# Performance work log

Measured on AMD Instinct MI355X. Metric: run time of the kernel, lower is better.

The kernel has to match this reference:

```python
import jax
jax.config.update('jax_enable_x64', True)
import jax.numpy as jnp
import numpy as np

N = 524288
C_IN = 64
C_OUT = 128
GRID = 1024
NB = 4
FILL_KEY = jnp.int64(1) << 62  # pad key, larger than any real packed key


def setup_inputs() -> dict:
    key = jax.random.key(0)
    k1, k2, k3, k4, k5, k6 = jax.random.split(key, 6)
    feat = jax.random.normal(k1, (N, C_IN), dtype=jnp.float32)
    coord = jax.random.uniform(k2, (N, 3), dtype=jnp.float32) * 100.0
    weight = jax.random.normal(k3, (C_OUT, C_IN), dtype=jnp.float32) / np.sqrt(C_IN)
    bias = jax.random.normal(k4, (C_OUT,), dtype=jnp.float32) * 0.01
    grid_coord = jax.random.randint(k5, (N, 3), 0, GRID, dtype=jnp.int64)
    batch = jnp.sort(jax.random.randint(k6, (N,), 0, NB, dtype=jnp.int64))
    return {"feat": feat, "coord": coord, "weight": weight, "bias": bias,
            "grid_coord": grid_coord, "batch": batch, "stride": 2}


def reference(feat, coord, weight, bias, grid_coord, batch, stride):
    n = feat.shape[0]
    g = grid_coord // stride                       # [N,3] int64
    packed = (g[:, 0] + (g[:, 1] << 16) + (g[:, 2] << 32) + (batch << 48))
    # sorted unique keys, padded at the end with FILL_KEY (fixed shape N)
    uniq = jnp.unique(packed, size=n, fill_value=FILL_KEY)
    cluster = jnp.searchsorted(uniq, packed)       # inverse indices [N]
    counts = jax.ops.segment_sum(jnp.ones((n,), jnp.float32), cluster, num_segments=n)
    valid = counts > 0
    # linear projection then max segment-reduce (equiv. to segment_csr 'max')
    proj = feat @ weight.T + bias                  # [N, C_OUT]
    seg_feat = jax.ops.segment_max(proj, cluster, num_segments=n)
    seg_feat = jnp.where(valid[:, None], seg_feat, 0.0)
    # mean segment-reduce of coords
    seg_coord = jax.ops.segment_sum(coord, cluster, num_segments=n)
    seg_coord = seg_coord / jnp.maximum(counts, 1.0)[:, None]
    # decode pooled grid coords and batch from the packed keys
    key_wo_b = jnp.where(valid, uniq % (jnp.int64(1) << 48), 0)
    gx = key_wo_b % (1 << 16)
    gy = (key_wo_b >> 16) % (1 << 16)
    gz = (key_wo_b >> 32) % (1 << 16)
    grid_out = jnp.stack([gx, gy, gz], axis=1)
    batch_out = jnp.where(valid, uniq >> 48, 0)
    return seg_feat, seg_coord, grid_out, batch_out, counts
```

## Files before the change

kernel.cpp:

```cpp
#include <hip/hip_runtime.h>
#include <stdint.h>

#define C_IN 64
#define C_OUT 128
#define NBUCK 32768
#define CAP 64

typedef unsigned int u32;
typedef unsigned long long u64;
typedef __attribute__((ext_vector_type(8))) short bf16x8;
typedef __attribute__((ext_vector_type(4))) float f32x4;

__device__ __forceinline__ bf16x8 cvt8(float4 a, float4 b) {
  union { bf16x8 v; __bf16 h[8]; } r;
  r.h[0] = (__bf16)a.x; r.h[1] = (__bf16)a.y;
  r.h[2] = (__bf16)a.z; r.h[3] = (__bf16)a.w;
  r.h[4] = (__bf16)b.x; r.h[5] = (__bf16)b.y;
  r.h[6] = (__bf16)b.z; r.h[7] = (__bf16)b.w;
  return r.v;
}

__global__ void k0_zero(uint4* __restrict__ p, int n4) {
  int i = blockIdx.x * blockDim.x + threadIdx.x;
  if (i < n4) p[i] = make_uint4(0u, 0u, 0u, 0u);
}

__global__ void k13_scatter(const int* __restrict__ grid, const int* __restrict__ batch,
                            const int* __restrict__ stride, int n,
                            u32* __restrict__ cnt, u64* __restrict__ pairsPad) {
  int q = blockIdx.x * blockDim.x + threadIdx.x;
  int base = q * 4;
  if (base >= n) return;
  int s = stride[0];
  u32 g[12], bt[4];
  if (base + 4 <= n) {
    const int4* g4 = (const int4*)grid;
    int4 ga = g4[q * 3], gb = g4[q * 3 + 1], gc = g4[q * 3 + 2];
    int4 bb = ((const int4*)batch)[q];
    g[0] = ga.x; g[1] = ga.y; g[2] = ga.z; g[3] = ga.w;
    g[4] = gb.x; g[5] = gb.y; g[6] = gb.z; g[7] = gb.w;
    g[8] = gc.x; g[9] = gc.y; g[10] = gc.z; g[11] = gc.w;
    bt[0] = bb.x; bt[1] = bb.y; bt[2] = bb.z; bt[3] = bb.w;
  } else {
    for (int j = 0; j < 12; j++) {
      int p = base * 3 + j;
      g[j] = (p < n * 3) ? (u32)grid[p] : 0u;
    }
    for (int j = 0; j < 4; j++) bt[j] = (base + j < n) ? (u32)batch[base + j] : 0u;
  }
#pragma unroll
  for (int j = 0; j < 4; j++) {
    int i = base + j;
    if (i >= n) break;
    u32 gx, gy, gz;
    if (s == 2) {
      gx = g[3 * j] >> 1; gy = g[3 * j + 1] >> 1; gz = g[3 * j + 2] >> 1;
    } else {
      gx = g[3 * j] / (u32)s; gy = g[3 * j + 1] / (u32)s; gz = g[3 * j + 2] / (u32)s;
    }
    u32 key = (bt[j] << 30) | (gz << 20) | (gy << 10) | gx;
    u32 bk = ((key >> 30) << 13) | (((key >> 20) & 0x1FFu) << 4) | ((key >> 15) & 0xFu);
    u32 pos = atomicAdd(&cnt[bk], 1u);
    if (pos < CAP) pairsPad[((size_t)bk << 6) | pos] = ((u64)key << 32) | (u32)i;
  }
}

__global__ __launch_bounds__(256) void k4_sort(u64* __restrict__ pairsPad,
                                               const u32* __restrict__ cnt,
                                               u32* __restrict__ bucketHeads) {
  int b = (blockIdx.x * blockDim.x + threadIdx.x) >> 6;
  int lane = threadIdx.x & 63;
  if (b >= NBUCK) return;
  u32 k = cnt[b];
  if (k > CAP) k = CAP;
  const u32 lo = (u32)b << 6;
  if (k == 0) { if (lane == 0) bucketHeads[b] = 0u; return; }
  if (k == 1) { if (lane == 0) bucketHeads[b] = 1u; return; }
  u64 v = (lane < (int)k) ? pairsPad[lo + lane] : ~0ull;
  u32 mykey = (u32)(v >> 32);
  int rank = 0, same_smaller = 0;
  for (u32 j = 0; j < k; j++) {
    u64 o = __shfl(v, (int)j, 64);
    bool lt = o < v;
    rank += lt ? 1 : 0;
    same_smaller += (lt && ((u32)(o >> 32) == mykey)) ? 1 : 0;
  }
  bool head = (lane < (int)k) && (same_smaller == 0);
  u64 hb = __ballot(head);
  if (lane < (int)k) pairsPad[lo + rank] = v;
  if (lane == 0) bucketHeads[b] = (u32)__popcll(hb);
}

__global__ void k2b_scan(const u32* __restrict__ bucketHeads, u32* __restrict__ segBase,
                         u32* __restrict__ meta) {
  __shared__ u32 part[1024];
  int t = threadIdx.x;
  const uint4* h4 = (const uint4*)bucketHeads;
  uint4 v[8];
  u32 s = 0;
#pragma unroll
  for (int q = 0; q < 8; q++) {
    v[q] = h4[t * 8 + q];
    s += v[q].x + v[q].y + v[q].z + v[q].w;
  }
  part[t] = s;
  __syncthreads();
  for (int d = 1; d < 1024; d <<= 1) {
    u32 x = (t >= d) ? part[t - d] : 0u;
    __syncthreads();
    part[t] += x;
    __syncthreads();
  }
  u32 run = part[t] - s;
  uint4* sb4 = (uint4*)segBase;
#pragma unroll
  for (int q = 0; q < 8; q++) {
    uint4 o;
    o.x = run; run += v[q].x;
    o.y = run; run += v[q].y;
    o.z = run; run += v[q].z;
    o.w = run; run += v[q].w;
    sb4[t * 8 + q] = o;
  }
  if (t == 1023) {
    meta[0] = run;
    meta[1] = 0u;
  }
}

__global__ __launch_bounds__(256) void k5_assign(
    const u64* __restrict__ pairsPad, const u32* __restrict__ cnt,
    const u32* __restrict__ segBase, const float* __restrict__ coord,
    u32* __restrict__ segStart, u32* __restrict__ cluster,
    float* __restrict__ out_grid, float* __restrict__ out_batch,
    float* __restrict__ out_coord, float* __restrict__ out_counts,
    u32* __restrict__ meta, u32* __restrict__ multiList) {
  int b = (blockIdx.x * blockDim.x + threadIdx.x) >> 6;
  int lane = threadIdx.x & 63;
  if (b >= NBUCK) return;
  u32 k = cnt[b];
  if (k > CAP) k = CAP;
  if (k == 0) return;
  const u32 lo = (u32)b << 6;
  bool inb = lane < (int)k;
  u64 v = inb ? pairsPad[lo + lane] : ~0ull;
  u32 mykey = (u32)(v >> 32);
  u32 idx = (u32)(v & 0xFFFFFFFFu);
  float cx = 0.f, cy = 0.f, cz = 0.f;
  if (inb) {
    cx = coord[(size_t)idx * 3 + 0];
    cy = coord[(size_t)idx * 3 + 1];
    cz = coord[(size_t)idx * 3 + 2];
  }
  u64 pv = __shfl_up(v, 1, 64);
  bool head = inb && (lane == 0 || (u32)(pv >> 32) != mykey);
  u64 hb = __ballot(head);
  u64 above = (lane < 63) ? (hb >> (lane + 1)) : 0ull;
#pragma unroll
  for (int d = 1; d < 64; d <<= 1) {
    float ox = __shfl_down(cx, d, 64);
    float oy = __shfl_down(cy, d, 64);
    float oz = __shfl_down(cz, d, 64);
    bool ok = (lane + d < 64) && ((above & ((1ull << d) - 1ull)) == 0ull);
    if (ok) { cx += ox; cy += oy; cz += oz; }
  }
  if (inb) {
    u32 seg = segBase[b] + (u32)__popcll(hb << (63 - lane)) - 1u;
    u32 cnt_run = above ? (u32)__builtin_ctzll(above) + 1u : (k - (u32)lane);
    bool multi_run = head ? (cnt_run > 1u) : true;
    cluster[idx] = seg | (multi_run ? 0x80000000u : 0u);
    if (head) {
      segStart[seg] = lo + (u32)lane;
      out_grid[(size_t)seg * 3 + 0] = (float)(mykey & 0x3FFu);
      out_grid[(size_t)seg * 3 + 1] = (float)((mykey >> 10) & 0x3FFu);
      out_grid[(size_t)seg * 3 + 2] = (float)((mykey >> 20) & 0x3FFu);
      out_batch[seg] = (float)(mykey >> 30);
      float fc = (float)cnt_run;
      out_counts[seg] = fc;
      out_coord[(size_t)seg * 3 + 0] = cx / fc;
      out_coord[(size_t)seg * 3 + 1] = cy / fc;
      out_coord[(size_t)seg * 3 + 2] = cz / fc;
      if (cnt_run > 1u) {
        u32 slot = atomicAdd(&meta[1], 1u);
        multiList[slot] = seg;
      }
    }
  }
}

__global__ __launch_bounds__(256) void k6_gemm(
    const float* __restrict__ feat, const float* __restrict__ weight,
    const float* __restrict__ bias, const u32* __restrict__ cluster,
    const u32* __restrict__ meta, float* __restrict__ out_feat,
    float* __restrict__ out_coord, float* __restrict__ out_grid,
    float* __restrict__ out_batch, float* __restrict__ out_counts, int n) {
  const int lane = threadIdx.x & 63;
  const int wid = threadIdx.x >> 6;
  const int col = lane & 15;
  const int h = lane >> 4;

  bf16x8 wf[8][2];
#pragma unroll
  for (int g = 0; g < 8; g++) {
    const float* wr = weight + (size_t)(g * 16 + col) * C_IN;
#pragma unroll
    for (int t = 0; t < 2; t++) {
      float4 a = *(const float4*)(wr + t * 32 + h * 8);
      float4 b = *(const float4*)(wr + t * 32 + h * 8 + 4);
      wf[g][t] = cvt8(a, b);
    }
  }
  float breg[8];
#pragma unroll
  for (int g = 0; g < 8; g++) breg[g] = bias[g * 16 + col];

  const int nmt = (n + 63) >> 6;
  for (int t = blockIdx.x * 4 + wid; t < nmt; t += gridDim.x * 4) {
    const int base = t << 6;
    float4 raw[4][4];
    u32 cme;
    if (base + 64 <= n) {
#pragma unroll
      for (int s = 0; s < 4; s++) {
        const float* fr = feat + (size_t)(base + s * 16 + col) * C_IN;
        raw[s][0] = *(const float4*)(fr + h * 8);
        raw[s][1] = *(const float4*)(fr + h * 8 + 4);
        raw[s][2] = *(const float4*)(fr + 32 + h * 8);
        raw[s][3] = *(const float4*)(fr + 32 + h * 8 + 4);
      }
      cme = cluster[base + lane];
    } else {
#pragma unroll
      for (int s = 0; s < 4; s++) {
        int p = base + s * 16 + col;
        if (p >= n) p = n - 1;
        const float* fr = feat + (size_t)p * C_IN;
        raw[s][0] = *(const float4*)(fr + h * 8);
        raw[s][1] = *(const float4*)(fr + h * 8 + 4);
        raw[s][2] = *(const float4*)(fr + 32 + h * 8);
        raw[s][3] = *(const float4*)(fr + 32 + h * 8 + 4);
      }
      cme = (base + lane < n) ? cluster[base + lane] : 0x80000000u;
    }
#pragma unroll
    for (int s = 0; s < 4; s++) {
      bf16x8 af0 = cvt8(raw[s][0], raw[s][1]);
      bf16x8 af1 = cvt8(raw[s][2], raw[s][3]);
      u32 cl[4];
#pragma unroll
      for (int i = 0; i < 4; i++) cl[i] = __shfl(cme, s * 16 + 4 * h + i, 64);
#pragma unroll
      for (int g = 0; g < 8; g++) {
        f32x4 acc = {0.f, 0.f, 0.f, 0.f};
        acc = __builtin_amdgcn_mfma_f32_16x16x32_bf16(af0, wf[g][0], acc, 0, 0, 0);
        acc = __builtin_amdgcn_mfma_f32_16x16x32_bf16(af1, wf[g][1], acc, 0, 0, 0);
#pragma unroll
        for (int i = 0; i < 4; i++) {
          if (!(cl[i] & 0x80000000u))
            __builtin_nontemporal_store(
                acc[i] + breg[g], &out_feat[(size_t)cl[i] * C_OUT + g * 16 + col]);
        }
      }
    }
  }

  u32 numSeg = meta[0];
  for (u32 r = numSeg + blockIdx.x; r < (u32)n; r += gridDim.x) {
    if (threadIdx.x < 32) {
      float4 z = {0.f, 0.f, 0.f, 0.f};
      ((float4*)(out_feat + (size_t)r * C_OUT))[threadIdx.x] = z;
    } else if (threadIdx.x == 32) {
      out_counts[r] = 0.f;
      out_batch[r] = 0.f;
    } else if (threadIdx.x == 33) {
      out_coord[(size_t)r * 3 + 0] = 0.f;
      out_coord[(size_t)r * 3 + 1] = 0.f;
      out_coord[(size_t)r * 3 + 2] = 0.f;
    } else if (threadIdx.x == 34) {
      out_grid[(size_t)r * 3 + 0] = 0.f;
      out_grid[(size_t)r * 3 + 1] = 0.f;
      out_grid[(size_t)r * 3 + 2] = 0.f;
    }
  }
}

__global__ __launch_bounds__(128) void k8_multi(
    const u64* __restrict__ pairsPad, const u32* __restrict__ segStart,
    const u32* __restrict__ meta, const u32* __restrict__ multiList,
    const float* __restrict__ out_counts, const float* __restrict__ feat,
    const float* __restrict__ weight, const float* __restrict__ bias,
    float* __restrict__ out_feat) {
  __shared__ float ldsF[C_IN];
  const int c = threadIdx.x;
  float wreg[C_IN];
  const float4* wrow = (const float4*)(weight + (size_t)c * C_IN);
#pragma unroll
  for (int q = 0; q < 16; q++) {
    float4 v = wrow[q];
    wreg[4 * q] = v.x; wreg[4 * q + 1] = v.y; wreg[4 * q + 2] = v.z; wreg[4 * q + 3] = v.w;
  }
  const float bc = bias[c];
  const u32 nm = meta[1];
  for (u32 m = blockIdx.x; m < nm; m += gridDim.x) {
    u32 seg = multiList[m];
    u32 st = segStart[seg];
    u32 en = st + (u32)out_counts[seg];
    float mx = -3.4e38f;
    for (u32 e = st; e < en; e++) {
      u32 idx = (u32)(pairsPad[e] & 0xFFFFFFFFu);
      __syncthreads();
      if (c < 16) ((float4*)ldsF)[c] = ((const float4*)(feat + (size_t)idx * C_IN))[c];
      __syncthreads();
      float d = bc;
#pragma unroll
      for (int q = 0; q < 16; q++) {
        float4 v = ((const float4*)ldsF)[q];
        d = fmaf(v.x, wreg[4 * q], d);
        d = fmaf(v.y, wreg[4 * q + 1], d);
        d = fmaf(v.z, wreg[4 * q + 2], d);
        d = fmaf(v.w, wreg[4 * q + 3], d);
      }
      mx = fmaxf(mx, d);
    }
    out_feat[(size_t)seg * C_OUT + c] = mx;
  }
}

extern "C" void kernel_launch(void* const* d_in, const int* in_sizes, int n_in,
                              void* d_out, int out_size, void* d_ws, size_t ws_size,
                              hipStream_t stream) {
  const float* feat = (const float*)d_in[0];
  const float* coord = (const float*)d_in[1];
  const float* weight = (const float*)d_in[2];
  const float* bias = (const float*)d_in[3];
  const int* grid = (const int*)d_in[4];
  const int* batch = (const int*)d_in[5];
  const int* stride = (const int*)d_in[6];
  const int n = in_sizes[0] / C_IN;

  float* out_feat = (float*)d_out;
  float* out_coord = out_feat + (size_t)n * C_OUT;
  float* out_grid = out_coord + (size_t)n * 3;
  float* out_batch = out_grid + (size_t)n * 3;
  float* out_counts = out_batch + n;

  u32* W = (u32*)d_ws;
  u32* cnt = W;
  u32* bucketHeads = W + 32768;
  u32* segBase = W + 65536;
  u32* meta = W + 98304;
  u32* segStart = W + 98368;
  u32* cluster = segStart + n;
  u32* multiList = cluster + n;
  size_t pe = 98368 + 2 * (size_t)n + 65536;
  pe = (pe + 1) & ~(size_t)1;
  u64* pairsPad = (u64*)(W + pe);

  int nb4 = (n / 4 + 255) / 256 + 1;
  k0_zero<<<32, 256, 0, stream>>>((uint4*)cnt, 32768 / 4);
  k13_scatter<<<nb4, 256, 0, stream>>>(grid, batch, stride, n, cnt, pairsPad);
  k4_sort<<<NBUCK / 4, 256, 0, stream>>>(pairsPad, cnt, bucketHeads);
  k2b_scan<<<1, 1024, 0, stream>>>(bucketHeads, segBase, meta);
  k5_assign<<<NBUCK / 4, 256, 0, stream>>>(pairsPad, cnt, segBase, coord, segStart, cluster,
                                           out_grid, out_batch, out_coord, out_counts,
                                           meta, multiList);
  k6_gemm<<<2048, 256, 0, stream>>>(feat, weight, bias, cluster, meta, out_feat,
                                    out_coord, out_grid, out_batch, out_counts, n);
  k8_multi<<<64, 128, 0, stream>>>(pairsPad, segStart, meta, multiList, out_counts,
                                   feat, weight, bias, out_feat);
}
```

Before: 180.3 us.

## Drive GEMM by output segment instead of input point, drop cluster array

The GEMM kernel now iterates over output segment rows. For singleton segments it gathers the single source point's features through segStart and pairsPad, and it writes zeros for padding rows itself, so the separate tail zero-fill of out_feat goes away. Output stores become contiguous per segment rather than scattered by a cluster index, and the cluster array is no longer written or read. In exchange, feature loads become indirect gathers with a dependent chain (out_counts, segStart, pairsPad), and tiles now cover 16 rows per wave instead of 64.

```diff
diff --git a/kernel.cpp b/kernel.cpp
--- a/kernel.cpp
+++ b/kernel.cpp
@@ -131,7 +131,7 @@
 __global__ __launch_bounds__(256) void k5_assign(
     const u64* __restrict__ pairsPad, const u32* __restrict__ cnt,
     const u32* __restrict__ segBase, const float* __restrict__ coord,
-    u32* __restrict__ segStart, u32* __restrict__ cluster,
+    u32* __restrict__ segStart,
     float* __restrict__ out_grid, float* __restrict__ out_batch,
     float* __restrict__ out_coord, float* __restrict__ out_counts,
     u32* __restrict__ meta, u32* __restrict__ multiList) {
@@ -164,36 +164,33 @@
     bool ok = (lane + d < 64) && ((above & ((1ull << d) - 1ull)) == 0ull);
     if (ok) { cx += ox; cy += oy; cz += oz; }
   }
-  if (inb) {
+  if (head) {
     u32 seg = segBase[b] + (u32)__popcll(hb << (63 - lane)) - 1u;
     u32 cnt_run = above ? (u32)__builtin_ctzll(above) + 1u : (k - (u32)lane);
-    bool multi_run = head ? (cnt_run > 1u) : true;
-    cluster[idx] = seg | (multi_run ? 0x80000000u : 0u);
-    if (head) {
-      segStart[seg] = lo + (u32)lane;
-      out_grid[(size_t)seg * 3 + 0] = (float)(mykey & 0x3FFu);
-      out_grid[(size_t)seg * 3 + 1] = (float)((mykey >> 10) & 0x3FFu);
-      out_grid[(size_t)seg * 3 + 2] = (float)((mykey >> 20) & 0x3FFu);
-      out_batch[seg] = (float)(mykey >> 30);
-      float fc = (float)cnt_run;
-      out_counts[seg] = fc;
-      out_coord[(size_t)seg * 3 + 0] = cx / fc;
-      out_coord[(size_t)seg * 3 + 1] = cy / fc;
-      out_coord[(size_t)seg * 3 + 2] = cz / fc;
-      if (cnt_run > 1u) {
-        u32 slot = atomicAdd(&meta[1], 1u);
-        multiList[slot] = seg;
-      }
+    segStart[seg] = lo + (u32)lane;
+    out_grid[(size_t)seg * 3 + 0] = (float)(mykey & 0x3FFu);
+    out_grid[(size_t)seg * 3 + 1] = (float)((mykey >> 10) & 0x3FFu);
+    out_grid[(size_t)seg * 3 + 2] = (float)((mykey >> 20) & 0x3FFu);
+    out_batch[seg] = (float)(mykey >> 30);
+    float fc = (float)cnt_run;
+    out_counts[seg] = fc;
+    out_coord[(size_t)seg * 3 + 0] = cx / fc;
+    out_coord[(size_t)seg * 3 + 1] = cy / fc;
+    out_coord[(size_t)seg * 3 + 2] = cz / fc;
+    if (cnt_run > 1u) {
+      u32 slot = atomicAdd(&meta[1], 1u);
+      multiList[slot] = seg;
     }
   }
 }
 
 __global__ __launch_bounds__(256) void k6_gemm(
     const float* __restrict__ feat, const float* __restrict__ weight,
-    const float* __restrict__ bias, const u32* __restrict__ cluster,
-    const u32* __restrict__ meta, float* __restrict__ out_feat,
-    float* __restrict__ out_coord, float* __restrict__ out_grid,
-    float* __restrict__ out_batch, float* __restrict__ out_counts, int n) {
+    const float* __restrict__ bias, const u64* __restrict__ pairsPad,
+    const u32* __restrict__ segStart, const u32* __restrict__ meta,
+    float* __restrict__ out_feat, float* __restrict__ out_coord,
+    float* __restrict__ out_grid, float* __restrict__ out_batch,
+    float* __restrict__ out_counts, int n) {
   const int lane = threadIdx.x & 63;
   const int wid = threadIdx.x >> 6;
   const int col = lane & 15;
@@ -214,69 +211,56 @@
 #pragma unroll
   for (int g = 0; g < 8; g++) breg[g] = bias[g * 16 + col];
 
-  const int nmt = (n + 63) >> 6;
-  for (int t = blockIdx.x * 4 + wid; t < nmt; t += gridDim.x * 4) {
-    const int base = t << 6;
-    float4 raw[4][4];
-    u32 cme;
-    if (base + 64 <= n) {
-#pragma unroll
-      for (int s = 0; s < 4; s++) {
-        const float* fr = feat + (size_t)(base + s * 16 + col) * C_IN;
-        raw[s][0] = *(const float4*)(fr + h * 8);
-        raw[s][1] = *(const float4*)(fr + h * 8 + 4);
-        raw[s][2] = *(const float4*)(fr + 32 + h * 8);
-        raw[s][3] = *(const float4*)(fr + 32 + h * 8 + 4);
+  const u32 numSeg = meta[0];
+  const int ntile = (n + 15) >> 4;
+  for (int t = blockIdx.x * 4 + wid; t < ntile; t += gridDim.x * 4) {
+    const int s0 = t << 4;
+    const u32 seg = (u32)(s0 + col);
+    u32 flag = 2u;
+    bf16x8 af0 = {}, af1 = {};
+    if (seg < numSeg) {
+      flag = 0u;
+      if (out_counts[seg] == 1.0f) {
+        flag = 1u;
+        u32 idx = (u32)(pairsPad[segStart[seg]] & 0xFFFFFFFFu);
+        const float* fr = feat + (size_t)idx * C_IN;
+        float4 a0 = *(const float4*)(fr + h * 8);
+        float4 a1 = *(const float4*)(fr + h * 8 + 4);
+        float4 a2 = *(const float4*)(fr + 32 + h * 8);
+        float4 a3 = *(const float4*)(fr + 32 + h * 8 + 4);
+        af0 = cvt8(a0, a1);
+        af1 = cvt8(a2, a3);
       }
-      cme = cluster[base + lane];
-    } else {
-#pragma unroll
-      for (int s = 0; s < 4; s++) {
-        int p = base + s * 16 + col;
-        if (p >= n) p = n - 1;
-        const float* fr = feat + (size_t)p * C_IN;
-        raw[s][0] = *(const float4*)(fr + h * 8);
-        raw[s][1] = *(const float4*)(fr + h * 8 + 4);
-        raw[s][2] = *(const float4*)(fr + 32 + h * 8);
-        raw[s][3] = *(const float4*)(fr + 32 + h * 8 + 4);
-      }
-      cme = (base + lane < n) ? cluster[base + lane] : 0x80000000u;
-    }
-#pragma unroll
-    for (int s = 0; s < 4; s++) {
-      bf16x8 af0 = cvt8(raw[s][0], raw[s][1]);
-      bf16x8 af1 = cvt8(raw[s][2], raw[s][3]);
-      u32 cl[4];
-#pragma unroll
-      for (int i = 0; i < 4; i++) cl[i] = __shfl(cme, s * 16 + 4 * h + i, 64);
-#pragma unroll
-      for (int g = 0; g < 8; g++) {
-        f32x4 acc = {0.f, 0.f, 0.f, 0.f};
-        acc = __builtin_amdgcn_mfma_f32_16x16x32_bf16(af0, wf[g][0], acc, 0, 0, 0);
-        acc = __builtin_amdgcn_mfma_f32_16x16x32_bf16(af1, wf[g][1], acc, 0, 0, 0);
-#pragma unroll
-        for (int i = 0; i < 4; i++) {
-          if (!(cl[i] & 0x80000000u))
-            __builtin_nontemporal_store(
-                acc[i] + breg[g], &out_feat[(size_t)cl[i] * C_OUT + g * 16 + col]);
+    }
+    u32 fl4[4];
+#pragma unroll
+    for (int i = 0; i < 4; i++) fl4[i] = __shfl(flag, 4 * h + i, 64);
+#pragma unroll
+    for (int g = 0; g < 8; g++) {
+      f32x4 acc = {0.f, 0.f, 0.f, 0.f};
+      acc = __builtin_amdgcn_mfma_f32_16x16x32_bf16(af0, wf[g][0], acc, 0, 0, 0);
+      acc = __builtin_amdgcn_mfma_f32_16x16x32_bf16(af1, wf[g][1], acc, 0, 0, 0);
+#pragma unroll
+      for (int i = 0; i < 4; i++) {
+        u32 f = fl4[i];
+        if (f) {
+          float vout = (f == 1u) ? (acc[i] + breg[g]) : 0.f;
+          __builtin_nontemporal_store(
+              vout, &out_feat[(size_t)(s0 + 4 * h + i) * C_OUT + g * 16 + col]);
         }
       }
     }
   }
 
-  u32 numSeg = meta[0];
   for (u32 r = numSeg + blockIdx.x; r < (u32)n; r += gridDim.x) {
-    if (threadIdx.x < 32) {
-      float4 z = {0.f, 0.f, 0.f, 0.f};
-      ((float4*)(out_feat + (size_t)r * C_OUT))[threadIdx.x] = z;
-    } else if (threadIdx.x == 32) {
+    if (threadIdx.x == 0) {
       out_counts[r] = 0.f;
       out_batch[r] = 0.f;
-    } else if (threadIdx.x == 33) {
+    } else if (threadIdx.x == 1) {
       out_coord[(size_t)r * 3 + 0] = 0.f;
       out_coord[(size_t)r * 3 + 1] = 0.f;
       out_coord[(size_t)r * 3 + 2] = 0.f;
-    } else if (threadIdx.x == 34) {
+    } else if (threadIdx.x == 2) {
       out_grid[(size_t)r * 3 + 0] = 0.f;
       out_grid[(size_t)r * 3 + 1] = 0.f;
       out_grid[(size_t)r * 3 + 2] = 0.f;
@@ -350,9 +334,8 @@
   u32* segBase = W + 65536;
   u32* meta = W + 98304;
   u32* segStart = W + 98368;
-  u32* cluster = segStart + n;
-  u32* multiList = cluster + n;
-  size_t pe = 98368 + 2 * (size_t)n + 65536;
+  u32* multiList = segStart + n;
+  size_t pe = 98368 + (size_t)n + 65536;
   pe = (pe + 1) & ~(size_t)1;
   u64* pairsPad = (u64*)(W + pe);
 
@@ -361,11 +344,11 @@
   k13_scatter<<<nb4, 256, 0, stream>>>(grid, batch, stride, n, cnt, pairsPad);
   k4_sort<<<NBUCK / 4, 256, 0, stream>>>(pairsPad, cnt, bucketHeads);
   k2b_scan<<<1, 1024, 0, stream>>>(bucketHeads, segBase, meta);
-  k5_assign<<<NBUCK / 4, 256, 0, stream>>>(pairsPad, cnt, segBase, coord, segStart, cluster,
+  k5_assign<<<NBUCK / 4, 256, 0, stream>>>(pairsPad, cnt, segBase, coord, segStart,
                                            out_grid, out_batch, out_coord, out_counts,
                                            meta, multiList);
-  k6_gemm<<<2048, 256, 0, stream>>>(feat, weight, bias, cluster, meta, out_feat,
-                                    out_coord, out_grid, out_batch, out_counts, n);
+  k6_gemm<<<2048, 256, 0, stream>>>(feat, weight, bias, pairsPad, segStart, meta,
+                                    out_feat, out_coord, out_grid, out_batch, out_counts, n);
   k8_multi<<<64, 128, 0, stream>>>(pairsPad, segStart, meta, multiList, out_counts,
                                    feat, weight, bias, out_feat);
 }
```

New measurement: 193.9 us. 1.08x slower.

## Iterate GEMM over output segments with gathered inputs instead of scattered outputs

Applied to the files above, without the earlier changes.

The GEMM kernel now walks output segment rows. For singleton segments it gathers the one input feature row through a new singleIdx array written by the assign kernel. Output stores become contiguous, padding rows are zeroed inside the GEMM tile loop, and the per-point cluster writes are dropped. The cost is that input feature reads become random gathers instead of sequential loads, and MFMA work is still done for multi-point and padding rows.

```diff
diff --git a/kernel.cpp b/kernel.cpp
--- a/kernel.cpp
+++ b/kernel.cpp
@@ -131,7 +131,7 @@
 __global__ __launch_bounds__(256) void k5_assign(
     const u64* __restrict__ pairsPad, const u32* __restrict__ cnt,
     const u32* __restrict__ segBase, const float* __restrict__ coord,
-    u32* __restrict__ segStart, u32* __restrict__ cluster,
+    u32* __restrict__ segStart, u32* __restrict__ singleIdx,
     float* __restrict__ out_grid, float* __restrict__ out_batch,
     float* __restrict__ out_coord, float* __restrict__ out_counts,
     u32* __restrict__ meta, u32* __restrict__ multiList) {
@@ -164,33 +164,30 @@
     bool ok = (lane + d < 64) && ((above & ((1ull << d) - 1ull)) == 0ull);
     if (ok) { cx += ox; cy += oy; cz += oz; }
   }
-  if (inb) {
+  if (head) {
     u32 seg = segBase[b] + (u32)__popcll(hb << (63 - lane)) - 1u;
     u32 cnt_run = above ? (u32)__builtin_ctzll(above) + 1u : (k - (u32)lane);
-    bool multi_run = head ? (cnt_run > 1u) : true;
-    cluster[idx] = seg | (multi_run ? 0x80000000u : 0u);
-    if (head) {
-      segStart[seg] = lo + (u32)lane;
-      out_grid[(size_t)seg * 3 + 0] = (float)(mykey & 0x3FFu);
-      out_grid[(size_t)seg * 3 + 1] = (float)((mykey >> 10) & 0x3FFu);
-      out_grid[(size_t)seg * 3 + 2] = (float)((mykey >> 20) & 0x3FFu);
-      out_batch[seg] = (float)(mykey >> 30);
-      float fc = (float)cnt_run;
-      out_counts[seg] = fc;
-      out_coord[(size_t)seg * 3 + 0] = cx / fc;
-      out_coord[(size_t)seg * 3 + 1] = cy / fc;
-      out_coord[(size_t)seg * 3 + 2] = cz / fc;
-      if (cnt_run > 1u) {
-        u32 slot = atomicAdd(&meta[1], 1u);
-        multiList[slot] = seg;
-      }
+    segStart[seg] = lo + (u32)lane;
+    singleIdx[seg] = (cnt_run == 1u) ? idx : 0xFFFFFFFFu;
+    out_grid[(size_t)seg * 3 + 0] = (float)(mykey & 0x3FFu);
+    out_grid[(size_t)seg * 3 + 1] = (float)((mykey >> 10) & 0x3FFu);
+    out_grid[(size_t)seg * 3 + 2] = (float)((mykey >> 20) & 0x3FFu);
+    out_batch[seg] = (float)(mykey >> 30);
+    float fc = (float)cnt_run;
+    out_counts[seg] = fc;
+    out_coord[(size_t)seg * 3 + 0] = cx / fc;
+    out_coord[(size_t)seg * 3 + 1] = cy / fc;
+    out_coord[(size_t)seg * 3 + 2] = cz / fc;
+    if (cnt_run > 1u) {
+      u32 slot = atomicAdd(&meta[1], 1u);
+      multiList[slot] = seg;
     }
   }
 }
 
 __global__ __launch_bounds__(256) void k6_gemm(
     const float* __restrict__ feat, const float* __restrict__ weight,
-    const float* __restrict__ bias, const u32* __restrict__ cluster,
+    const float* __restrict__ bias, const u32* __restrict__ singleIdx,
     const u32* __restrict__ meta, float* __restrict__ out_feat,
     float* __restrict__ out_coord, float* __restrict__ out_grid,
     float* __restrict__ out_batch, float* __restrict__ out_counts, int n) {
@@ -214,41 +211,40 @@
 #pragma unroll
   for (int g = 0; g < 8; g++) breg[g] = bias[g * 16 + col];
 
+  const u32 numSeg = meta[0];
   const int nmt = (n + 63) >> 6;
   for (int t = blockIdx.x * 4 + wid; t < nmt; t += gridDim.x * 4) {
-    const int base = t << 6;
+    const int s0 = t << 6;
+    const int myseg = s0 + lane;
+    u32 sidx = 0xFFFFFFFFu;
+    u32 flag = 0u;
+    if (myseg < n) {
+      if ((u32)myseg < numSeg) {
+        sidx = singleIdx[myseg];
+        flag = (sidx != 0xFFFFFFFFu) ? 1u : 0u;
+      } else {
+        flag = 2u;
+      }
+    }
     float4 raw[4][4];
-    u32 cme;
-    if (base + 64 <= n) {
-#pragma unroll
-      for (int s = 0; s < 4; s++) {
-        const float* fr = feat + (size_t)(base + s * 16 + col) * C_IN;
-        raw[s][0] = *(const float4*)(fr + h * 8);
-        raw[s][1] = *(const float4*)(fr + h * 8 + 4);
-        raw[s][2] = *(const float4*)(fr + 32 + h * 8);
-        raw[s][3] = *(const float4*)(fr + 32 + h * 8 + 4);
-      }
-      cme = cluster[base + lane];
-    } else {
-#pragma unroll
-      for (int s = 0; s < 4; s++) {
-        int p = base + s * 16 + col;
-        if (p >= n) p = n - 1;
-        const float* fr = feat + (size_t)p * C_IN;
-        raw[s][0] = *(const float4*)(fr + h * 8);
-        raw[s][1] = *(const float4*)(fr + h * 8 + 4);
-        raw[s][2] = *(const float4*)(fr + 32 + h * 8);
-        raw[s][3] = *(const float4*)(fr + 32 + h * 8 + 4);
-      }
-      cme = (base + lane < n) ? cluster[base + lane] : 0x80000000u;
+#pragma unroll
+    for (int s = 0; s < 4; s++) {
+      u32 rflag = __shfl(flag, s * 16 + col, 64);
+      u32 ridx = __shfl(sidx, s * 16 + col, 64);
+      if (rflag != 1u) ridx = 0u;
+      const float* fr = feat + (size_t)ridx * C_IN;
+      raw[s][0] = *(const float4*)(fr + h * 8);
+      raw[s][1] = *(const float4*)(fr + h * 8 + 4);
+      raw[s][2] = *(const float4*)(fr + 32 + h * 8);
+      raw[s][3] = *(const float4*)(fr + 32 + h * 8 + 4);
     }
 #pragma unroll
     for (int s = 0; s < 4; s++) {
       bf16x8 af0 = cvt8(raw[s][0], raw[s][1]);
       bf16x8 af1 = cvt8(raw[s][2], raw[s][3]);
-      u32 cl[4];
-#pragma unroll
-      for (int i = 0; i < 4; i++) cl[i] = __shfl(cme, s * 16 + 4 * h + i, 64);
+      u32 fl4[4];
+#pragma unroll
+      for (int i = 0; i < 4; i++) fl4[i] = __shfl(flag, s * 16 + 4 * h + i, 64);
 #pragma unroll
       for (int g = 0; g < 8; g++) {
         f32x4 acc = {0.f, 0.f, 0.f, 0.f};
@@ -256,27 +252,27 @@
         acc = __builtin_amdgcn_mfma_f32_16x16x32_bf16(af1, wf[g][1], acc, 0, 0, 0);
 #pragma unroll
         for (int i = 0; i < 4; i++) {
-          if (!(cl[i] & 0x80000000u))
+          u32 f = fl4[i];
+          if (f) {
+            float vout = (f == 1u) ? (acc[i] + breg[g]) : 0.f;
             __builtin_nontemporal_store(
-                acc[i] + breg[g], &out_feat[(size_t)cl[i] * C_OUT + g * 16 + col]);
+                vout,
+                &out_feat[(size_t)(s0 + s * 16 + 4 * h + i) * C_OUT + g * 16 + col]);
+          }
         }
       }
     }
   }
 
-  u32 numSeg = meta[0];
   for (u32 r = numSeg + blockIdx.x; r < (u32)n; r += gridDim.x) {
-    if (threadIdx.x < 32) {
-      float4 z = {0.f, 0.f, 0.f, 0.f};
-      ((float4*)(out_feat + (size_t)r * C_OUT))[threadIdx.x] = z;
-    } else if (threadIdx.x == 32) {
+    if (threadIdx.x == 0) {
       out_counts[r] = 0.f;
       out_batch[r] = 0.f;
-    } else if (threadIdx.x == 33) {
+    } else if (threadIdx.x == 1) {
       out_coord[(size_t)r * 3 + 0] = 0.f;
       out_coord[(size_t)r * 3 + 1] = 0.f;
       out_coord[(size_t)r * 3 + 2] = 0.f;
-    } else if (threadIdx.x == 34) {
+    } else if (threadIdx.x == 2) {
       out_grid[(size_t)r * 3 + 0] = 0.f;
       out_grid[(size_t)r * 3 + 1] = 0.f;
       out_grid[(size_t)r * 3 + 2] = 0.f;
@@ -350,8 +346,8 @@
   u32* segBase = W + 65536;
   u32* meta = W + 98304;
   u32* segStart = W + 98368;
-  u32* cluster = segStart + n;
-  u32* multiList = cluster + n;
+  u32* singleIdx = segStart + n;
+  u32* multiList = singleIdx + n;
   size_t pe = 98368 + 2 * (size_t)n + 65536;
   pe = (pe + 1) & ~(size_t)1;
   u64* pairsPad = (u64*)(W + pe);
@@ -361,10 +357,10 @@
   k13_scatter<<<nb4, 256, 0, stream>>>(grid, batch, stride, n, cnt, pairsPad);
   k4_sort<<<NBUCK / 4, 256, 0, stream>>>(pairsPad, cnt, bucketHeads);
   k2b_scan<<<1, 1024, 0, stream>>>(bucketHeads, segBase, meta);
-  k5_assign<<<NBUCK / 4, 256, 0, stream>>>(pairsPad, cnt, segBase, coord, segStart, cluster,
+  k5_assign<<<NBUCK / 4, 256, 0, stream>>>(pairsPad, cnt, segBase, coord, segStart, singleIdx,
                                            out_grid, out_batch, out_coord, out_counts,
                                            meta, multiList);
-  k6_gemm<<<2048, 256, 0, stream>>>(feat, weight, bias, cluster, meta, out_feat,
+  k6_gemm<<<2048, 256, 0, stream>>>(feat, weight, bias, singleIdx, meta, out_feat,
                                     out_coord, out_grid, out_batch, out_counts, n);
   k8_multi<<<64, 128, 0, stream>>>(pairsPad, segStart, meta, multiList, out_counts,
                                    feat, weight, bias, out_feat);
```

New measurement: 176.5 us. -2.1%, faster.
